# Kernel tuning notes

Measured on AMD Instinct MI355X. Metric: run time of the kernel, lower is better.

The kernel has to match this reference:

```python
import jax, jax.numpy as jnp
from jax import lax
import numpy as np

F_IN, F_OUT, T = 32, 64, 8
H1 = (3 * F_IN + F_OUT) // 4  # 40
H2 = F_OUT                    # 64
N, E = 50000, 800000


def setup_inputs() -> dict:
    key = jax.random.key(0)
    ks = jax.random.split(key, 8)
    def p(k, shape, fan_in):
        return jax.random.normal(k, shape, jnp.float32) / np.float32(np.sqrt(fan_in))
    return {
        "temporal_features": jax.random.normal(ks[0], (N, F_IN, T), jnp.float32),
        "src": jax.random.randint(ks[1], (E,), 0, N, jnp.int32),
        "dst": jax.random.randint(ks[2], (E,), 0, N, jnp.int32),
        "W1": p(ks[3], (F_IN, H1), F_IN), "b1": jnp.zeros((H1,), jnp.float32),
        "W2": p(ks[4], (H1, H2), H1),   "b2": jnp.zeros((H2,), jnp.float32),
        "W3": p(ks[5], (H2, F_OUT), H2), "b3": jnp.zeros((F_OUT,), jnp.float32),
        "Wc": p(ks[6], (F_OUT, F_OUT, 3), F_OUT * 3),  # Conv1d weight [out, in, k]
        "bc": jnp.zeros((F_OUT,), jnp.float32),
    }


def _graph_conv(h, src, dst, out_norm, in_norm, W, b, act, n):
    # dgl GraphConv, norm='both': D_out^{-1/2} -> sum-aggregate -> D_in^{-1/2} -> linear
    h = h * out_norm[:, None, None]                       # [N, t, f]
    agg = jax.ops.segment_sum(h[src], dst, num_segments=n)  # irregular gather/scatter
    h = agg * in_norm[:, None, None]
    h = jnp.einsum("nti,io->nto", h, W) + b
    return jax.nn.relu(h) if act else h


def reference(temporal_features, src, dst, W1, b1, W2, b2, W3, b3, Wc, bc):
    n = temporal_features.shape[0]
    ones = jnp.ones(src.shape, temporal_features.dtype)
    out_deg = jax.ops.segment_sum(ones, src, num_segments=n)
    in_deg = jax.ops.segment_sum(ones, dst, num_segments=n)
    out_norm = jnp.clip(out_deg, 1.0, None) ** -0.5
    in_norm = jnp.clip(in_deg, 1.0, None) ** -0.5

    h = jnp.swapaxes(temporal_features, -2, -1)  # [N, t, f_in]
    h = _graph_conv(h, src, dst, out_norm, in_norm, W1, b1, True, n)
    h = _graph_conv(h, src, dst, out_norm, in_norm, W2, b2, True, n)
    h = _graph_conv(h, src, dst, out_norm, in_norm, W3, b3, False, n)
    h = jnp.swapaxes(h, -2, -1)  # [N, f_out, t]

    out = lax.conv_general_dilated(
        h, Wc, window_strides=(1,), padding=((1, 1),),
        dimension_numbers=("NCH", "OIH", "NCH"))
    return out + bc[None, :, None]
```

## Files before the change

### kernel.cpp

```cpp
#include <hip/hip_runtime.h>

typedef float f32x4 __attribute__((ext_vector_type(4)));


__global__ __launch_bounds__(256) void deg_kernel(const int* __restrict__ src,
                                                  const int* __restrict__ dst,
                                                  int* __restrict__ out_deg,
                                                  int* __restrict__ in_deg, int E) {
  int e = blockIdx.x * 256 + threadIdx.x;
  if (e < E) {
    atomicAdd(&out_deg[src[e]], 1);
    atomicAdd(&in_deg[dst[e]], 1);
  }
}

__global__ __launch_bounds__(256) void norm_kernel(const int* __restrict__ out_deg,
                                                   const int* __restrict__ in_deg,
                                                   float* __restrict__ out_norm,
                                                   float* __restrict__ in_norm, int N) {
  int n = blockIdx.x * 256 + threadIdx.x;
  if (n < N) {
    out_norm[n] = 1.0f / sqrtf((float)max(out_deg[n], 1));
    in_norm[n]  = 1.0f / sqrtf((float)max(in_deg[n], 1));
  }
}

__global__ __launch_bounds__(256) void wct_kernel(const float* __restrict__ Wc,
                                                  float* __restrict__ wct) {
  int m = blockIdx.x * 256 + threadIdx.x;
  if (m < 12288) wct[m] = Wc[(m & 63) * 192 + (m >> 6)];
}


__global__ __launch_bounds__(256) void scan_partial_kernel(const int* __restrict__ deg,
                                                           int* __restrict__ partial, int N) {
  __shared__ int ws[4];
  int tid = threadIdx.x, lane = tid & 63, wv = tid >> 6;
  int base = blockIdx.x * 1024;
  int v = 0;
#pragma unroll
  for (int k = 0; k < 4; ++k) {
    int i = base + tid + k * 256;
    if (i < N) v += deg[i];
  }
  for (int d = 32; d > 0; d >>= 1) v += __shfl_down(v, d, 64);
  if (lane == 0) ws[wv] = v;
  __syncthreads();
  if (tid == 0) partial[blockIdx.x] = ws[0] + ws[1] + ws[2] + ws[3];
}

__global__ __launch_bounds__(1024) void scan_partials_kernel(int* __restrict__ partial, int P) {
  __shared__ int wsum[16];
  int tid = threadIdx.x, lane = tid & 63, wv = tid >> 6;
  int v = (tid < P) ? partial[tid] : 0;
  int x = v;
  for (int d = 1; d < 64; d <<= 1) {
    int y = __shfl_up(x, d, 64);
    if (lane >= d) x += y;
  }
  if (lane == 63) wsum[wv] = x;
  __syncthreads();
  if (wv == 0 && lane < 16) {
    int y = wsum[lane];
    int z = y;
    for (int d = 1; d < 16; d <<= 1) {
      int q = __shfl_up(z, d, 64);
      if (lane >= d) z += q;
    }
    wsum[lane] = z - y;
  }
  __syncthreads();
  if (tid < P) partial[tid] = wsum[wv] + x - v;
}

__global__ __launch_bounds__(1024) void scan_apply_kernel(const int* __restrict__ deg,
                                                          const int* __restrict__ partial,
                                                          int* __restrict__ off, int N) {
  __shared__ int wsum[16];
  int tid = threadIdx.x, lane = tid & 63, wv = tid >> 6;
  int i = blockIdx.x * 1024 + tid;
  int v = (i < N) ? deg[i] : 0;
  int x = v;
  for (int d = 1; d < 64; d <<= 1) {
    int y = __shfl_up(x, d, 64);
    if (lane >= d) x += y;
  }
  if (lane == 63) wsum[wv] = x;
  __syncthreads();
  if (wv == 0 && lane < 16) {
    int y = wsum[lane];
    int z = y;
    for (int d = 1; d < 16; d <<= 1) {
      int q = __shfl_up(z, d, 64);
      if (lane >= d) z += q;
    }
    wsum[lane] = z - y;
  }
  __syncthreads();
  int excl = partial[blockIdx.x] + wsum[wv] + (x - v);
  if (i < N) off[i] = excl;
  if (i == N - 1) off[N] = excl + v;
}

__global__ __launch_bounds__(256) void scatter_kernel(const int* __restrict__ src,
                                                      const int* __restrict__ dst,
                                                      const int* __restrict__ in_off,
                                                      int* __restrict__ cursor,
                                                      int* __restrict__ csr_src, int E) {
  int e = blockIdx.x * 256 + threadIdx.x;
  if (e < E) {
    int d = dst[e];
    int p = atomicAdd(&cursor[d], 1);
    csr_src[in_off[d] + p] = src[e];
  }
}

template <int NC>
__device__ __forceinline__ void keepalive(f32x4* v) {
#pragma unroll
  for (int k = 0; k < NC; ++k) asm volatile("" : "+v"(v[k]));
}

template <int F_IN, int F_OUT, int TS, int L, bool IT_LAYOUT, bool RELU,
          bool GNORM, bool SCALE_OUT>
__device__ __forceinline__ void layer_body(
    const float* __restrict__ h_in, const int* __restrict__ csr_src,
    const int* __restrict__ in_off, const float* __restrict__ out_norm,
    const float* __restrict__ in_norm, const float* __restrict__ W,
    const float* __restrict__ bias, float* __restrict__ h_out, int N) {
  constexpr int NF4 = F_IN * 2;
  constexpr int NC = NF4 / L;
  constexpr int M = 64 / L;
  constexpr int SLOTS = 4 * M;
  constexpr int SLOT = (IT_LAYOUT ? F_IN * 8 : TS * 8) + 8;
  __shared__ float agg[SLOTS][SLOT];
  int tid = threadIdx.x;
  int wave = tid >> 6, lane = tid & 63;
  int q = lane / L, r = lane % L;
  int slot = wave * M + q;
  int n = blockIdx.x * SLOTS + slot;
  bool valid = (n < N);

  f32x4 acc[NC];
#pragma unroll
  for (int k = 0; k < NC; ++k) acc[k] = (f32x4){0.f, 0.f, 0.f, 0.f};

  if (valid) {
    int e0 = in_off[n], e1 = in_off[n + 1];
    const f32x4* h4 = (const f32x4*)h_in;
    int j = e0;
    if (e1 - e0 >= 2) {
      int sA = csr_src[j], sB = csr_src[j + 1];
      do {
        int cA = sA, cB = sB;
        int jn = j + 2;
        sA = csr_src[min(jn, e1 - 1)];
        sB = csr_src[min(jn + 1, e1 - 1)];
        float wA = 1.f, wB = 1.f;
        if constexpr (GNORM) { wA = out_norm[cA]; wB = out_norm[cB]; }
        const f32x4* pA = h4 + (size_t)cA * NF4 + r;
        const f32x4* pB = h4 + (size_t)cB * NF4 + r;
        f32x4 vA[NC], vB[NC];
#pragma unroll
        for (int k = 0; k < NC; ++k) vA[k] = pA[k * L];
#pragma unroll
        for (int k = 0; k < NC; ++k) vB[k] = pB[k * L];
        keepalive<NC>(vA);
        keepalive<NC>(vB);
#pragma unroll
        for (int k = 0; k < NC; ++k)
#pragma unroll
          for (int e = 0; e < 4; ++e) acc[k][e] = fmaf(vA[k][e], wA, acc[k][e]);
#pragma unroll
        for (int k = 0; k < NC; ++k)
#pragma unroll
          for (int e = 0; e < 4; ++e) acc[k][e] = fmaf(vB[k][e], wB, acc[k][e]);
        j = jn;
      } while (j + 2 <= e1);
    }
    if (j < e1) {
      int s = csr_src[j];
      float w = 1.f;
      if constexpr (GNORM) w = out_norm[s];
      const f32x4* p = h4 + (size_t)s * NF4 + r;
#pragma unroll
      for (int k = 0; k < NC; ++k) {
        f32x4 v = p[k * L];
#pragma unroll
        for (int e = 0; e < 4; ++e) acc[k][e] = fmaf(v[e], w, acc[k][e]);
      }
    }
    float innm = in_norm[n];
#pragma unroll
    for (int k = 0; k < NC; ++k) {
      int el = (k * L + r) * 4;
      int addr;
      if constexpr (IT_LAYOUT) {
        addr = el;
      } else {
        int t = el / F_IN;
        int i = el - t * F_IN;
        addr = t * TS + i;
      }
      *(f32x4*)&agg[slot][addr] = acc[k] * innm;
    }
  }

  constexpr int G = F_OUT / 8;
  int t = lane >> 3, og = lane & 7;
  float acc2[M][G];
  {
    float bb[G];
    if constexpr (G == 8) {
      float4 bA = *(const float4*)&bias[og * 8];
      float4 bB = *(const float4*)&bias[og * 8 + 4];
      bb[0] = bA.x; bb[1] = bA.y; bb[2] = bA.z; bb[3] = bA.w;
      bb[4] = bB.x; bb[5] = bB.y; bb[6] = bB.z; bb[7] = bB.w;
    } else {
#pragma unroll
      for (int c = 0; c < G; ++c) bb[c] = bias[og * G + c];
    }
#pragma unroll
    for (int qq = 0; qq < M; ++qq)
#pragma unroll
      for (int c = 0; c < G; ++c) acc2[qq][c] = bb[c];
  }
#pragma unroll 4
  for (int i = 0; i < F_IN; ++i) {
    float wrow[G];
    if constexpr (G == 8) {
      float4 wA = *(const float4*)&W[i * F_OUT + og * 8];
      float4 wB = *(const float4*)&W[i * F_OUT + og * 8 + 4];
      wrow[0] = wA.x; wrow[1] = wA.y; wrow[2] = wA.z; wrow[3] = wA.w;
      wrow[4] = wB.x; wrow[5] = wB.y; wrow[6] = wB.z; wrow[7] = wB.w;
    } else {
#pragma unroll
      for (int c = 0; c < G; ++c) wrow[c] = W[i * F_OUT + og * G + c];
    }
    int raddr;
    if constexpr (IT_LAYOUT) raddr = i * 8 + t;
    else raddr = t * TS + i;
#pragma unroll
    for (int qq = 0; qq < M; ++qq) {
      float a = agg[wave * M + qq][raddr];
#pragma unroll
      for (int c = 0; c < G; ++c) acc2[qq][c] = fmaf(a, wrow[c], acc2[qq][c]);
    }
  }
#pragma unroll
  for (int qq = 0; qq < M; ++qq) {
    int n2 = blockIdx.x * SLOTS + wave * M + qq;
    if (n2 < N) {
      float osc = 1.f;
      if constexpr (SCALE_OUT) osc = out_norm[n2];
      float res[G];
#pragma unroll
      for (int c = 0; c < G; ++c) {
        float v = acc2[qq][c];
        if constexpr (RELU) v = fmaxf(v, 0.f);
        res[c] = v * osc;
      }
      float* orow = h_out + (size_t)n2 * (F_OUT * 8) + t * F_OUT + og * G;
      if constexpr (G == 8) {
        *(float4*)&orow[0] = make_float4(res[0], res[1], res[2], res[3]);
        *(float4*)&orow[4] = make_float4(res[4], res[5], res[6], res[7]);
      } else {
#pragma unroll
        for (int c = 0; c < G; ++c) orow[c] = res[c];
      }
    }
  }
}

__global__ __launch_bounds__(256, 7) void layer1_k(
    const float* __restrict__ h_in, const int* __restrict__ csr_src,
    const int* __restrict__ in_off, const float* __restrict__ out_norm,
    const float* __restrict__ in_norm, const float* __restrict__ W,
    const float* __restrict__ bias, float* __restrict__ h_out, int N) {
  layer_body<32, 40, 0, 16, true, true, true, true>(
      h_in, csr_src, in_off, out_norm, in_norm, W, bias, h_out, N);
}

__global__ __launch_bounds__(256, 6) void layer2_k(
    const float* __restrict__ h_in, const int* __restrict__ csr_src,
    const int* __restrict__ in_off, const float* __restrict__ out_norm,
    const float* __restrict__ in_norm, const float* __restrict__ W,
    const float* __restrict__ bias, float* __restrict__ h_out, int N) {
  layer_body<40, 64, 44, 16, false, true, false, true>(
      h_in, csr_src, in_off, out_norm, in_norm, W, bias, h_out, N);
}

__global__ __launch_bounds__(256, 4) void layer3_conv_k(
    const float* __restrict__ h_in, const int* __restrict__ csr_src,
    const int* __restrict__ in_off, const float* __restrict__ in_norm,
    const float* __restrict__ W, const float* __restrict__ bias,
    const float* __restrict__ wct, const float* __restrict__ bc,
    float* __restrict__ out, int N) {
  constexpr int SLOT = 8 * 68 + 8;
  __shared__ float agg[16][SLOT];
  int tid = threadIdx.x;
  int wave = tid >> 6, lane = tid & 63;
  int q = lane >> 4, r = lane & 15;
  int slot = wave * 4 + q;
  int n = blockIdx.x * 16 + slot;
  bool valid = (n < N);

  f32x4 acc[8];
#pragma unroll
  for (int k = 0; k < 8; ++k) acc[k] = (f32x4){0.f, 0.f, 0.f, 0.f};

  if (valid) {
    int e0 = in_off[n], e1 = in_off[n + 1];
    const f32x4* h4 = (const f32x4*)h_in;
    int j = e0;
    if (e1 - e0 >= 2) {
      int sA = csr_src[j], sB = csr_src[j + 1];
      do {
        int cA = sA, cB = sB;
        int jn = j + 2;
        sA = csr_src[min(jn, e1 - 1)];
        sB = csr_src[min(jn + 1, e1 - 1)];
        const f32x4* pA = h4 + (size_t)cA * 128 + r;
        const f32x4* pB = h4 + (size_t)cB * 128 + r;
        f32x4 vA[8], vB[8];
#pragma unroll
        for (int k = 0; k < 8; ++k) vA[k] = pA[k * 16];
#pragma unroll
        for (int k = 0; k < 8; ++k) vB[k] = pB[k * 16];
        keepalive<8>(vA);
        keepalive<8>(vB);
#pragma unroll
        for (int k = 0; k < 8; ++k) acc[k] += vA[k];
#pragma unroll
        for (int k = 0; k < 8; ++k) acc[k] += vB[k];
        j = jn;
      } while (j + 2 <= e1);
    }
    if (j < e1) {
      int s = csr_src[j];
      const f32x4* p = h4 + (size_t)s * 128 + r;
#pragma unroll
      for (int k = 0; k < 8; ++k) acc[k] += p[k * 16];
    }
    float innm = in_norm[n];
#pragma unroll
    for (int k = 0; k < 8; ++k) {
      int addr = k * 68 + (r << 2);
      *(f32x4*)&agg[slot][addr] = acc[k] * innm;
    }
  }

  int t = lane >> 3, og = lane & 7;
  float acc2[4][8];
  {
    float4 bA = *(const float4*)&bias[og * 8];
    float4 bB = *(const float4*)&bias[og * 8 + 4];
    float bb[8] = {bA.x, bA.y, bA.z, bA.w, bB.x, bB.y, bB.z, bB.w};
#pragma unroll
    for (int qq = 0; qq < 4; ++qq)
#pragma unroll
      for (int c = 0; c < 8; ++c) acc2[qq][c] = bb[c];
  }
#pragma unroll 4
  for (int i = 0; i < 64; ++i) {
    float4 wA = *(const float4*)&W[i * 64 + og * 8];
    float4 wB = *(const float4*)&W[i * 64 + og * 8 + 4];
    float wrow[8] = {wA.x, wA.y, wA.z, wA.w, wB.x, wB.y, wB.z, wB.w};
    int raddr = t * 68 + i;
#pragma unroll
    for (int qq = 0; qq < 4; ++qq) {
      float a = agg[wave * 4 + qq][raddr];
#pragma unroll
      for (int c = 0; c < 8; ++c) acc2[qq][c] = fmaf(a, wrow[c], acc2[qq][c]);
    }
  }

#pragma unroll
  for (int qq = 0; qq < 4; ++qq) {
    float* sb = &agg[wave * 4 + qq][og * 64 + t];
#pragma unroll
    for (int c = 0; c < 8; ++c) sb[((c + og) & 7) << 3] = acc2[qq][c];
  }

  float4 b4 = *(const float4*)&bc[r * 4];
  float bcv[4] = {b4.x, b4.y, b4.z, b4.w};
  float cacc[4][8];
#pragma unroll
  for (int c = 0; c < 4; ++c)
#pragma unroll
    for (int tt = 0; tt < 8; ++tt) cacc[c][tt] = bcv[c];

  const float4* wct4 = (const float4*)wct;
  const float* hq = &agg[slot][0];
#pragma unroll 2
  for (int i = 0; i < 64; ++i) {
    int ib = i >> 3, ic = i & 7;
    const float* hi = &hq[ib * 64 + (((ic + ib) & 7) << 3)];
    float4 hA = *(const float4*)hi;
    float4 hB = *(const float4*)(hi + 4);
    float4 w0 = wct4[(i * 3 + 0) * 16 + r];
    float4 w1 = wct4[(i * 3 + 1) * 16 + r];
    float4 w2 = wct4[(i * 3 + 2) * 16 + r];
    float h[8] = {hA.x, hA.y, hA.z, hA.w, hB.x, hB.y, hB.z, hB.w};
    float wk0[4] = {w0.x, w0.y, w0.z, w0.w};
    float wk1[4] = {w1.x, w1.y, w1.z, w1.w};
    float wk2[4] = {w2.x, w2.y, w2.z, w2.w};
#pragma unroll
    for (int c = 0; c < 4; ++c) {
#pragma unroll
      for (int tt = 0; tt < 8; ++tt) cacc[c][tt] = fmaf(wk1[c], h[tt], cacc[c][tt]);
#pragma unroll
      for (int tt = 1; tt < 8; ++tt) cacc[c][tt] = fmaf(wk0[c], h[tt - 1], cacc[c][tt]);
#pragma unroll
      for (int tt = 0; tt < 7; ++tt) cacc[c][tt] = fmaf(wk2[c], h[tt + 1], cacc[c][tt]);
    }
  }
  if (valid) {
    float* ob = out + (size_t)n * 512 + r * 32;
#pragma unroll
    for (int c = 0; c < 4; ++c) {
      *(float4*)&ob[c * 8] = make_float4(cacc[c][0], cacc[c][1], cacc[c][2], cacc[c][3]);
      *(float4*)&ob[c * 8 + 4] = make_float4(cacc[c][4], cacc[c][5], cacc[c][6], cacc[c][7]);
    }
  }
}


extern "C" void kernel_launch(void* const* d_in, const int* in_sizes, int n_in,
                              void* d_out, int out_size, void* d_ws, size_t ws_size,
                              hipStream_t stream) {
  const float* tf = (const float*)d_in[0];
  const int* src = (const int*)d_in[1];
  const int* dst = (const int*)d_in[2];
  const float* W1 = (const float*)d_in[3];
  const float* b1 = (const float*)d_in[4];
  const float* W2 = (const float*)d_in[5];
  const float* b2 = (const float*)d_in[6];
  const float* W3 = (const float*)d_in[7];
  const float* b3 = (const float*)d_in[8];
  const float* Wc = (const float*)d_in[9];
  const float* bc = (const float*)d_in[10];

  int N = in_sizes[0] / 256;
  int E = in_sizes[1];

  char* ws = (char*)d_ws;
  size_t pos = 0;
  auto alloc = [&](size_t bytes) -> void* {
    void* p = ws + pos;
    pos += (bytes + 255) & ~(size_t)255;
    return p;
  };
  int* in_deg   = (int*)alloc((size_t)N * 4);
  int* out_deg  = (int*)alloc((size_t)N * 4);
  int* cursor   = (int*)alloc((size_t)N * 4);
  int* in_off   = (int*)alloc((size_t)(N + 1) * 4);
  int* partial  = (int*)alloc((size_t)1024 * 4);
  float* o_norm = (float*)alloc((size_t)N * 4);
  float* i_norm = (float*)alloc((size_t)N * 4);
  int* csr      = (int*)alloc((size_t)E * 4);
  float* wct    = (float*)alloc((size_t)12288 * 4);
  float* h1     = (float*)alloc((size_t)N * 320 * 4);
  float* h2     = (float*)alloc((size_t)N * 512 * 4);

  hipMemsetAsync(in_deg, 0, (size_t)((char*)in_off - (char*)in_deg), stream);

  deg_kernel<<<(E + 255) / 256, 256, 0, stream>>>(src, dst, out_deg, in_deg, E);
  norm_kernel<<<(N + 255) / 256, 256, 0, stream>>>(out_deg, in_deg, o_norm, i_norm, N);
  wct_kernel<<<48, 256, 0, stream>>>(Wc, wct);

  int P = (N + 1023) / 1024;
  scan_partial_kernel<<<P, 256, 0, stream>>>(in_deg, partial, N);
  scan_partials_kernel<<<1, 1024, 0, stream>>>(partial, P);
  scan_apply_kernel<<<P, 1024, 0, stream>>>(in_deg, partial, in_off, N);

  scatter_kernel<<<(E + 255) / 256, 256, 0, stream>>>(src, dst, in_off, cursor, csr, E);

  layer1_k<<<(N + 15) / 16, 256, 0, stream>>>(tf, csr, in_off, o_norm, i_norm, W1, b1, h1, N);
  layer2_k<<<(N + 15) / 16, 256, 0, stream>>>(h1, csr, in_off, o_norm, i_norm, W2, b2, h2, N);
  layer3_conv_k<<<(N + 15) / 16, 256, 0, stream>>>(h2, csr, in_off, i_norm, W3, b3,
                                                   wct, bc, (float*)d_out, N);
}
```

Baseline: 803.7 us.

## Software-pipeline neighbor gathers with ping-pong buffers and adjust occupancy hints

Replaces the 2-at-a-time gather loop, which relied on asm keepalive barriers, with a ping-pong software pipeline. The next neighbor's row load is issued before the current one is accumulated, so memory latency overlaps with the FMAs. Launch-bound occupancy hints become amdgpu_waves_per_eu attributes. Layer 2's shared-memory row stride drops from 44 to 40 floats, which may raise LDS bank conflicts. Dropping the csr_src prefetch means each index load now sits directly on the dependency chain before its row gather.

New measurement: 1.340 ms. 1.67x slower.

```diff
diff --git a/kernel.cpp b/kernel.cpp
--- a/kernel.cpp
+++ b/kernel.cpp
@@ -113,12 +113,6 @@
     int p = atomicAdd(&cursor[d], 1);
     csr_src[in_off[d] + p] = src[e];
   }
-}
-
-template <int NC>
-__device__ __forceinline__ void keepalive(f32x4* v) {
-#pragma unroll
-  for (int k = 0; k < NC; ++k) asm volatile("" : "+v"(v[k]));
 }
 
 template <int F_IN, int F_OUT, int TS, int L, bool IT_LAYOUT, bool RELU,
@@ -148,46 +142,55 @@
   if (valid) {
     int e0 = in_off[n], e1 = in_off[n + 1];
     const f32x4* h4 = (const f32x4*)h_in;
-    int j = e0;
-    if (e1 - e0 >= 2) {
-      int sA = csr_src[j], sB = csr_src[j + 1];
-      do {
-        int cA = sA, cB = sB;
-        int jn = j + 2;
-        sA = csr_src[min(jn, e1 - 1)];
-        sB = csr_src[min(jn + 1, e1 - 1)];
-        float wA = 1.f, wB = 1.f;
-        if constexpr (GNORM) { wA = out_norm[cA]; wB = out_norm[cB]; }
-        const f32x4* pA = h4 + (size_t)cA * NF4 + r;
-        const f32x4* pB = h4 + (size_t)cB * NF4 + r;
-        f32x4 vA[NC], vB[NC];
+    if (e1 > e0) {
+      f32x4 vA[NC], vB[NC];
+      int sA = csr_src[e0];
+      float wA = 1.f;
+      if constexpr (GNORM) wA = out_norm[sA];
+      {
+        const f32x4* pA = h4 + (size_t)sA * NF4 + r;
 #pragma unroll
         for (int k = 0; k < NC; ++k) vA[k] = pA[k * L];
-#pragma unroll
-        for (int k = 0; k < NC; ++k) vB[k] = pB[k * L];
-        keepalive<NC>(vA);
-        keepalive<NC>(vB);
-#pragma unroll
-        for (int k = 0; k < NC; ++k)
-#pragma unroll
-          for (int e = 0; e < 4; ++e) acc[k][e] = fmaf(vA[k][e], wA, acc[k][e]);
-#pragma unroll
-        for (int k = 0; k < NC; ++k)
-#pragma unroll
-          for (int e = 0; e < 4; ++e) acc[k][e] = fmaf(vB[k][e], wB, acc[k][e]);
-        j = jn;
-      } while (j + 2 <= e1);
-    }
-    if (j < e1) {
-      int s = csr_src[j];
-      float w = 1.f;
-      if constexpr (GNORM) w = out_norm[s];
-      const f32x4* p = h4 + (size_t)s * NF4 + r;
-#pragma unroll
-      for (int k = 0; k < NC; ++k) {
-        f32x4 v = p[k * L];
-#pragma unroll
-        for (int e = 0; e < 4; ++e) acc[k][e] = fmaf(v[e], w, acc[k][e]);
+      }
+      int k = e0;
+      while (true) {
+        if (k + 1 < e1) {
+          int sB = csr_src[k + 1];
+          float wB = 1.f;
+          if constexpr (GNORM) wB = out_norm[sB];
+          const f32x4* pB = h4 + (size_t)sB * NF4 + r;
+#pragma unroll
+          for (int c = 0; c < NC; ++c) vB[c] = pB[c * L];
+#pragma unroll
+          for (int c = 0; c < NC; ++c)
+#pragma unroll
+            for (int e = 0; e < 4; ++e) acc[c][e] = fmaf(vA[c][e], wA, acc[c][e]);
+          if (k + 2 < e1) {
+            int sA2 = csr_src[k + 2];
+            float wA2 = 1.f;
+            if constexpr (GNORM) wA2 = out_norm[sA2];
+            const f32x4* pA2 = h4 + (size_t)sA2 * NF4 + r;
+#pragma unroll
+            for (int c = 0; c < NC; ++c) vA[c] = pA2[c * L];
+            wA = wA2;
+#pragma unroll
+            for (int c = 0; c < NC; ++c)
+#pragma unroll
+              for (int e = 0; e < 4; ++e) acc[c][e] = fmaf(vB[c][e], wB, acc[c][e]);
+            k += 2;
+            continue;
+          }
+#pragma unroll
+          for (int c = 0; c < NC; ++c)
+#pragma unroll
+            for (int e = 0; e < 4; ++e) acc[c][e] = fmaf(vB[c][e], wB, acc[c][e]);
+          break;
+        }
+#pragma unroll
+        for (int c = 0; c < NC; ++c)
+#pragma unroll
+          for (int e = 0; e < 4; ++e) acc[c][e] = fmaf(vA[c][e], wA, acc[c][e]);
+        break;
       }
     }
     float innm = in_norm[n];
@@ -272,7 +275,8 @@
   }
 }
 
-__global__ __launch_bounds__(256, 7) void layer1_k(
+__global__ __launch_bounds__(256)
+__attribute__((amdgpu_waves_per_eu(7, 7))) void layer1_k(
     const float* __restrict__ h_in, const int* __restrict__ csr_src,
     const int* __restrict__ in_off, const float* __restrict__ out_norm,
     const float* __restrict__ in_norm, const float* __restrict__ W,
@@ -281,16 +285,18 @@
       h_in, csr_src, in_off, out_norm, in_norm, W, bias, h_out, N);
 }
 
-__global__ __launch_bounds__(256, 6) void layer2_k(
+__global__ __launch_bounds__(256)
+__attribute__((amdgpu_waves_per_eu(6, 6))) void layer2_k(
     const float* __restrict__ h_in, const int* __restrict__ csr_src,
     const int* __restrict__ in_off, const float* __restrict__ out_norm,
     const float* __restrict__ in_norm, const float* __restrict__ W,
     const float* __restrict__ bias, float* __restrict__ h_out, int N) {
-  layer_body<40, 64, 44, 16, false, true, false, true>(
+  layer_body<40, 64, 40, 16, false, true, false, true>(
       h_in, csr_src, in_off, out_norm, in_norm, W, bias, h_out, N);
 }
 
-__global__ __launch_bounds__(256, 4) void layer3_conv_k(
+__global__ __launch_bounds__(256)
+__attribute__((amdgpu_waves_per_eu(4, 4))) void layer3_conv_k(
     const float* __restrict__ h_in, const int* __restrict__ csr_src,
     const int* __restrict__ in_off, const float* __restrict__ in_norm,
     const float* __restrict__ W, const float* __restrict__ bias,
@@ -312,35 +318,41 @@
   if (valid) {
     int e0 = in_off[n], e1 = in_off[n + 1];
     const f32x4* h4 = (const f32x4*)h_in;
-    int j = e0;
-    if (e1 - e0 >= 2) {
-      int sA = csr_src[j], sB = csr_src[j + 1];
-      do {
-        int cA = sA, cB = sB;
-        int jn = j + 2;
-        sA = csr_src[min(jn, e1 - 1)];
-        sB = csr_src[min(jn + 1, e1 - 1)];
-        const f32x4* pA = h4 + (size_t)cA * 128 + r;
-        const f32x4* pB = h4 + (size_t)cB * 128 + r;
-        f32x4 vA[8], vB[8];
-#pragma unroll
-        for (int k = 0; k < 8; ++k) vA[k] = pA[k * 16];
-#pragma unroll
-        for (int k = 0; k < 8; ++k) vB[k] = pB[k * 16];
-        keepalive<8>(vA);
-        keepalive<8>(vB);
-#pragma unroll
-        for (int k = 0; k < 8; ++k) acc[k] += vA[k];
-#pragma unroll
-        for (int k = 0; k < 8; ++k) acc[k] += vB[k];
-        j = jn;
-      } while (j + 2 <= e1);
-    }
-    if (j < e1) {
-      int s = csr_src[j];
-      const f32x4* p = h4 + (size_t)s * 128 + r;
-#pragma unroll
-      for (int k = 0; k < 8; ++k) acc[k] += p[k * 16];
+    if (e1 > e0) {
+      f32x4 vA[8], vB[8];
+      {
+        int sA = csr_src[e0];
+        const f32x4* pA = h4 + (size_t)sA * 128 + r;
+#pragma unroll
+        for (int c = 0; c < 8; ++c) vA[c] = pA[c * 16];
+      }
+      int k = e0;
+      while (true) {
+        if (k + 1 < e1) {
+          int sB = csr_src[k + 1];
+          const f32x4* pB = h4 + (size_t)sB * 128 + r;
+#pragma unroll
+          for (int c = 0; c < 8; ++c) vB[c] = pB[c * 16];
+#pragma unroll
+          for (int c = 0; c < 8; ++c) acc[c] += vA[c];
+          if (k + 2 < e1) {
+            int sA2 = csr_src[k + 2];
+            const f32x4* pA2 = h4 + (size_t)sA2 * 128 + r;
+#pragma unroll
+            for (int c = 0; c < 8; ++c) vA[c] = pA2[c * 16];
+#pragma unroll
+            for (int c = 0; c < 8; ++c) acc[c] += vB[c];
+            k += 2;
+            continue;
+          }
+#pragma unroll
+          for (int c = 0; c < 8; ++c) acc[c] += vB[c];
+          break;
+        }
+#pragma unroll
+        for (int c = 0; c < 8; ++c) acc[c] += vA[c];
+        break;
+      }
     }
     float innm = in_norm[n];
 #pragma unroll
```
